# Performance work log

Hardware: AMD Instinct MI355X
Metric: run time of the kernel (lower is better)

Reference implementation:

```python
import jax, jax.numpy as jnp
import numpy as np

B, C_IN, C_OUT, N, K = 8, 64, 128, 2048, 16
EPS = 1e-5  # torch BatchNorm2d default


def setup_inputs() -> dict:
    key = jax.random.key(0)
    ks = jax.random.split(key, 2)
    x = jax.random.normal(ks[0], (B, C_IN, N, 1), dtype=jnp.float32)
    # Conv2d(2*C_IN, C_OUT, 1) kaiming_normal weight, zero bias; 1x1 kernel -> [C_OUT, 2*C_IN]
    W = jax.random.normal(ks[1], (C_OUT, 2 * C_IN), dtype=jnp.float32) * np.float32(np.sqrt(2.0 / (2 * C_IN)))
    b = jnp.zeros((C_OUT,), jnp.float32)
    gamma = jnp.ones((C_OUT,), jnp.float32)   # BN weight filled with 1
    beta = jnp.zeros((C_OUT,), jnp.float32)   # BN bias zeroed
    return {"x": x, "W": W, "b": b, "gamma": gamma, "beta": beta, "k": K}


def reference(x, W, b, gamma, beta, k):
    # x: [B, C, N, 1]
    xs = x[..., 0]                              # [B, C, N]
    feats = jnp.transpose(xs, (0, 2, 1))        # [B, N, C]
    # knn: pairwise_distance = -||xi||^2 + 2 xi.xj - ||xj||^2 (negative sq dist)
    sq = jnp.sum(xs * xs, axis=1)               # [B, N]
    gram = jnp.einsum('bcn,bcm->bnm', xs, xs)   # [B, N, N]
    pd = 2.0 * gram - sq[:, :, None] - sq[:, None, :]
    idx = jax.lax.top_k(pd, k)[1]               # [B, N, k] neighbor indices
    # gather: x_j = neighbor features, x_i = center features broadcast over k
    x_j = jnp.take_along_axis(feats[:, None, :, :], idx[:, :, :, None], axis=2)  # [B, N, k, C]
    x_i = feats[:, :, None, :]                  # [B, N, 1, C]
    e = jnp.concatenate([jnp.broadcast_to(x_i, x_j.shape), x_j - x_i], axis=-1)  # [B, N, k, 2C]
    # 1x1 conv (matmul over channels) + ReLU
    h = jax.nn.relu(jnp.einsum('bnkc,oc->bnko', e, W) + b)  # [B, N, k, O]
    # BatchNorm2d in training mode: batch stats over (B, N, k), biased variance
    mean = jnp.mean(h, axis=(0, 1, 2))
    var = jnp.mean(jnp.square(h - mean), axis=(0, 1, 2))
    h = (h - mean) * jax.lax.rsqrt(var + EPS) * gamma + beta
    # max over neighbors, back to [B, O, N, 1]
    out = jnp.max(h, axis=2)                    # [B, N, O]
    return jnp.transpose(out, (0, 2, 1))[..., None]
```

## Files before the change

### kernel.cpp

```cpp
#include <hip/hip_runtime.h>
#include <math.h>

#define BB 8
#define CIN 64
#define CO 128
#define NPT 2048
#define KK 16
#define EPSV 1e-5f
#define LOSCALE 2048.0f

typedef unsigned int u32;
typedef unsigned long long u64;
typedef _Float16 f16x8 __attribute__((ext_vector_type(8)));
typedef float f32x4 __attribute__((ext_vector_type(4)));

__global__ __launch_bounds__(256) void k_prep_pv(
    const float* __restrict__ x, const float* __restrict__ W,
    const float* __restrict__ bias, float* __restrict__ sq,
    _Float16* __restrict__ xh, _Float16* __restrict__ xl,
    float* __restrict__ p, float* __restrict__ v) {
  __shared__ float tile[64][65];
  __shared__ float tileT[64][68];
  __shared__ float psum[4][64];
  int bid = blockIdx.x;
  int b = bid >> 5;
  int n0 = (bid & 31) << 6;
  int tid = threadIdx.x;
  int q = tid >> 6, lo = tid & 63;
#pragma unroll
  for (int i = 0; i < 16; ++i) {
    int c = i * 4 + q;
    tile[c][lo] = x[((size_t)(b * CIN + c)) * NPT + n0 + lo];
  }
  __syncthreads();
  float ps = 0.f;
#pragma unroll
  for (int i = 0; i < 16; ++i) {
    float t = tile[q * 16 + i][lo];
    ps += t * t;
  }
  psum[q][lo] = ps;
#pragma unroll
  for (int i = 0; i < 16; ++i) {
    int ni = i * 4 + q;
    float val = tile[lo][ni];
    tileT[ni][lo] = val;
    size_t o = ((size_t)(b * NPT + n0 + ni)) * CIN + lo;
    _Float16 h = (_Float16)val;
    xh[o] = h;
    xl[o] = (_Float16)((val - (float)h) * LOSCALE);
  }
  __syncthreads();
  if (q == 0) {
    sq[(size_t)b * NPT + n0 + lo] = psum[0][lo] + psum[1][lo] + psum[2][lo] + psum[3][lo];
  }
  int o = tid & 127, hh = tid >> 7;
  const float4* W1 = (const float4*)&W[o * 2 * CIN];
  const float4* W2 = (const float4*)&W[o * 2 * CIN + CIN];
  float bo = bias[o];
#pragma unroll 2
  for (int t = 0; t < 32; ++t) {
    int node = t * 2 + hh;
    float a1 = 0.f, a2 = 0.f;
#pragma unroll
    for (int c4 = 0; c4 < 16; ++c4) {
      float4 xv = *(const float4*)&tileT[node][c4 * 4];
      float4 w1 = W1[c4];
      float4 w2 = W2[c4];
      a1 += xv.x * w1.x + xv.y * w1.y + xv.z * w1.z + xv.w * w1.w;
      a2 += xv.x * w2.x + xv.y * w2.y + xv.z * w2.z + xv.w * w2.w;
    }
    size_t gn = ((size_t)(b * NPT + n0 + node)) * CO + o;
    p[gn] = a1 - a2 + bo;
    v[gn] = a2;
  }
}

__global__ __launch_bounds__(1024) void k_dist_topk(
    const _Float16* __restrict__ xh, const _Float16* __restrict__ xl,
    const float* __restrict__ sq, int* __restrict__ idxout) {
  __shared__ uint4 tiles[16][2][256];
  __shared__ float submax[16][64];
  __shared__ float2 cand[16][96];
  __shared__ int cnt[16];
  __shared__ float tauf[16];

  int bid = (blockIdx.x & 7) * 128 + (blockIdx.x >> 3);
  int b = bid >> 7;
  int rt = (bid & 127) << 4;
  int tid = threadIdx.x;
  int w = tid >> 6, lane = tid & 63;
  int lr = lane & 15, lg = lane >> 4;
  const _Float16* xhb = xh + (size_t)b * NPT * CIN;
  const _Float16* xlb = xl + (size_t)b * NPT * CIN;
  const float* sqb = sq + (size_t)b * NPT;

  if (tid < 16) cnt[tid] = 0;

  const size_t arow = (size_t)(rt + lr) * CIN + lg * 8;
  f16x8 ah0 = *(const f16x8*)(xhb + arow);
  f16x8 ah1 = *(const f16x8*)(xhb + arow + 32);
  f16x8 al0 = *(const f16x8*)(xlb + arow);
  f16x8 al1 = *(const f16x8*)(xlb + arow + 32);
  float4 sqr = *(const float4*)(sqb + rt + lg * 4);
  float sqrv[4] = {sqr.x, sqr.y, sqr.z, sqr.w};
  float csqs[8];
#pragma unroll
  for (int t = 0; t < 8; ++t) csqs[t] = sqb[(w * 8 + t) * 16 + lr];

  const char* xhB = (const char*)xhb;
  const char* xlB = (const char*)xlb;
  const int su = (lane ^ ((lane >> 3) & 7)) * 16;

#define ISSUE_TILE(T)                                                          \
  {                                                                            \
    const int tb_ = (w * 8 + (T)) * 2048;                                      \
    uint4* buf_ = &tiles[w][(T) & 1][0];                                       \
    __builtin_amdgcn_global_load_lds((const uint4*)(xhB + tb_ + su),           \
                                     buf_, 16, 0, 0);                          \
    __builtin_amdgcn_global_load_lds((const uint4*)(xhB + tb_ + 1024 + su),    \
                                     buf_ + 64, 16, 0, 0);                     \
    __builtin_amdgcn_global_load_lds((const uint4*)(xlB + tb_ + su),           \
                                     buf_ + 128, 16, 0, 0);                    \
    __builtin_amdgcn_global_load_lds((const uint4*)(xlB + tb_ + 1024 + su),    \
                                     buf_ + 192, 16, 0, 0);                    \
  }

  ISSUE_TILE(0)
  ISSUE_TILE(1)

  const int uh0 = lr * 8 + (lg ^ (lr & 7));
  const int uh1 = lr * 8 + ((lg + 4) ^ (lr & 7));
  float vals[32];

#pragma unroll
  for (int t = 0; t < 8; ++t) {
    if (t < 7) { asm volatile("s_waitcnt vmcnt(4)" ::: "memory"); }
    else       { asm volatile("s_waitcnt vmcnt(0)" ::: "memory"); }
    __builtin_amdgcn_sched_barrier(0);
    const uint4* bufr = &tiles[w][t & 1][0];
    f16x8 bh0 = *(const f16x8*)(bufr + uh0);
    f16x8 bh1 = *(const f16x8*)(bufr + uh1);
    f16x8 bl0 = *(const f16x8*)(bufr + 128 + uh0);
    f16x8 bl1 = *(const f16x8*)(bufr + 128 + uh1);
    asm volatile("s_waitcnt lgkmcnt(0)" ::: "memory");
    __builtin_amdgcn_sched_barrier(0);
    if (t == 0) ISSUE_TILE(2)
    if (t == 1) ISSUE_TILE(3)
    if (t == 2) ISSUE_TILE(4)
    if (t == 3) ISSUE_TILE(5)
    if (t == 4) ISSUE_TILE(6)
    if (t == 5) ISSUE_TILE(7)
    f32x4 acc0 = {0.f, 0.f, 0.f, 0.f};
    f32x4 acc1 = {0.f, 0.f, 0.f, 0.f};
    acc1 = __builtin_amdgcn_mfma_f32_16x16x32_f16(ah0, bl0, acc1, 0, 0, 0);
    acc1 = __builtin_amdgcn_mfma_f32_16x16x32_f16(al0, bh0, acc1, 0, 0, 0);
    acc1 = __builtin_amdgcn_mfma_f32_16x16x32_f16(ah1, bl1, acc1, 0, 0, 0);
    acc1 = __builtin_amdgcn_mfma_f32_16x16x32_f16(al1, bh1, acc1, 0, 0, 0);
    acc0 = __builtin_amdgcn_mfma_f32_16x16x32_f16(ah0, bh0, acc0, 0, 0, 0);
    acc0 = __builtin_amdgcn_mfma_f32_16x16x32_f16(ah1, bh1, acc0, 0, 0, 0);
    const float k2 = 2.0f / LOSCALE;
#pragma unroll
    for (int q = 0; q < 4; ++q) {
      vals[t * 4 + q] = fmaf(acc1[q], k2, 2.f * acc0[q]) - (sqrv[q] + csqs[t]);
    }
  }
#undef ISSUE_TILE

  float rmax[4];
#pragma unroll
  for (int q = 0; q < 4; ++q) {
    float m = vals[q];
#pragma unroll
    for (int t = 1; t < 8; ++t) m = fmaxf(m, vals[t * 4 + q]);
    m = fmaxf(m, __shfl_xor(m, 1, 64));
    m = fmaxf(m, __shfl_xor(m, 2, 64));
    rmax[q] = m;
  }
  if ((lr & 3) == 0) {
    int pool = w * 4 + (lr >> 2);
#pragma unroll
    for (int q = 0; q < 4; ++q) submax[lg * 4 + q][pool] = rmax[q];
  }
  __syncthreads();

  {
    u32 ou = __float_as_uint(submax[w][lane]);
    ou = (ou & 0x80000000u) ? ~ou : (ou | 0x80000000u);
    u32 lo = 0u;
#pragma unroll
    for (int s2 = 31; s2 >= 16; --s2) {
      u32 cd = lo | (1u << s2);
      u64 bal = __ballot(ou >= cd);
      if (__popcll(bal) >= KK) lo = cd;
    }
    u32 tb = (lo & 0x80000000u) ? (lo ^ 0x80000000u) : ~lo;
    if (lane == 0) tauf[w] = __uint_as_float(tb);
  }
  __syncthreads();

  {
    float tq[4];
#pragma unroll
    for (int q = 0; q < 4; ++q) tq[q] = tauf[lg * 4 + q];
#pragma unroll
    for (int t = 0; t < 8; ++t) {
#pragma unroll
      for (int q = 0; q < 4; ++q) {
        float vv = vals[t * 4 + q];
        if (vv >= tq[q]) {
          int r = lg * 4 + q;
          int pos = atomicAdd(&cnt[r], 1);
          if (pos < 96) cand[r][pos] = make_float2(vv, __int_as_float((w * 8 + t) * 16 + lr));
        }
      }
    }
  }
  __syncthreads();

  int total = cnt[w];
  if (total > 96) total = 96;
  const float NINF = -__builtin_inff();
  float cv = NINF;
  int ci = 0x7FFFFFFF;
  int n1 = total < 64 ? total : 64;
  if (lane < n1) {
    float2 pr = cand[w][lane];
    cv = pr.x; ci = __float_as_int(pr.y);
  }

#define PSORT(KMAX)                                                        \
  _Pragma("unroll") for (int k = 2; k <= (KMAX); k <<= 1) {                \
    _Pragma("unroll") for (int j = k >> 1; j > 0; j >>= 1) {               \
      float pv = __shfl_xor(cv, j, 64);                                    \
      int pi = __shfl_xor(ci, j, 64);                                      \
      bool up = (lane & k) != 0;                                           \
      bool lw = (lane & j) == 0;                                           \
      bool gt = (cv > pv) || (cv == pv && ci < pi);                        \
      bool keep = (lw != up) ? gt : !gt;                                   \
      cv = keep ? cv : pv;                                                 \
      ci = keep ? ci : pi;                                                 \
    }                                                                      \
  }

  if (total > 32) {
    PSORT(64)
    if (total > 64) {
      if (lane >= 16) {
        int src2 = 48 + lane;
        if (src2 < total) {
          float2 pr = cand[w][src2];
          cv = pr.x; ci = __float_as_int(pr.y);
        } else { cv = NINF; ci = 0x7FFFFFFF; }
      }
      PSORT(64)
    }
  } else {
    PSORT(32)
  }
#undef PSORT

  if (lane < KK) idxout[((size_t)(b * NPT + rt + w)) * KK + lane] = ci;
}

__global__ __launch_bounds__(256) void k_stats(
    const float* __restrict__ p, const float* __restrict__ v,
    const int* __restrict__ idx, float* __restrict__ psums,
    float* __restrict__ psqs, float* __restrict__ mxb) {
  __shared__ float rs[8][CO];
  __shared__ float rq[8][CO];
  int bid = (blockIdx.x & 7) * 128 + (blockIdx.x >> 3);
  int b = bid >> 7;
  int n0 = (bid & 127) << 4;
  int tid = threadIdx.x;
  int o4 = tid & 31, ns = tid >> 5;
  const float* vb = v + (size_t)b * NPT * CO;
  float4 s = {0.f, 0.f, 0.f, 0.f};
  float4 qq = {0.f, 0.f, 0.f, 0.f};
#pragma unroll 1
  for (int g = 0; g < 2; ++g) {
    int gn = b * NPT + n0 + g * 8 + ns;
    size_t po = (size_t)gn * CO + o4 * 4;
    float4 p4 = *(const float4*)(p + po);
    const int* id = idx + (size_t)gn * KK;
    int4 j0 = *(const int4*)(id);
    int4 j1 = *(const int4*)(id + 4);
    int4 j2 = *(const int4*)(id + 8);
    int4 j3 = *(const int4*)(id + 12);
    int jj[16] = {j0.x, j0.y, j0.z, j0.w, j1.x, j1.y, j1.z, j1.w,
                  j2.x, j2.y, j2.z, j2.w, j3.x, j3.y, j3.z, j3.w};
    float4 mx4 = {-1e30f, -1e30f, -1e30f, -1e30f};
#pragma unroll
    for (int k = 0; k < KK; ++k) {
      float4 v4 = *(const float4*)(vb + (size_t)jj[k] * CO + o4 * 4);
      float h0 = fmaxf(p4.x + v4.x, 0.f);
      float h1 = fmaxf(p4.y + v4.y, 0.f);
      float h2 = fmaxf(p4.z + v4.z, 0.f);
      float h3 = fmaxf(p4.w + v4.w, 0.f);
      s.x += h0; s.y += h1; s.z += h2; s.w += h3;
      qq.x += h0 * h0; qq.y += h1 * h1; qq.z += h2 * h2; qq.w += h3 * h3;
      mx4.x = fmaxf(mx4.x, h0); mx4.y = fmaxf(mx4.y, h1);
      mx4.z = fmaxf(mx4.z, h2); mx4.w = fmaxf(mx4.w, h3);
    }
    *(float4*)(mxb + po) = mx4;
  }
  rs[ns][o4 * 4 + 0] = s.x;  rs[ns][o4 * 4 + 1] = s.y;
  rs[ns][o4 * 4 + 2] = s.z;  rs[ns][o4 * 4 + 3] = s.w;
  rq[ns][o4 * 4 + 0] = qq.x; rq[ns][o4 * 4 + 1] = qq.y;
  rq[ns][o4 * 4 + 2] = qq.z; rq[ns][o4 * 4 + 3] = qq.w;
  __syncthreads();
  if (tid < CO) {
    float ts = 0.f, tq = 0.f;
#pragma unroll
    for (int i = 0; i < 8; ++i) { ts += rs[i][tid]; tq += rq[i][tid]; }
    psums[(size_t)bid * CO + tid] = ts;
    psqs[(size_t)bid * CO + tid] = tq;
  }
}

__global__ __launch_bounds__(64) void k_final(
    const float* __restrict__ psums, const float* __restrict__ psqs,
    const float* __restrict__ gamma, const float* __restrict__ beta,
    float* __restrict__ scale, float* __restrict__ shift) {
  int o = blockIdx.x;
  int t = threadIdx.x;
  float s = 0.f, q = 0.f;
  for (int i = t; i < BB * (NPT / 16); i += 64) {
    s += psums[(size_t)i * CO + o];
    q += psqs[(size_t)i * CO + o];
  }
#pragma unroll
  for (int d = 32; d >= 1; d >>= 1) {
    s += __shfl_down(s, d, 64);
    q += __shfl_down(q, d, 64);
  }
  if (t == 0) {
    const float M = (float)(BB * NPT * KK);
    float mean = s / M;
    float var = q / M - mean * mean;
    float sc = gamma[o] * rsqrtf(var + EPSV);
    scale[o] = sc;
    shift[o] = beta[o] - mean * sc;
  }
}

__global__ __launch_bounds__(256) void k_out_fast(
    const float* __restrict__ mxb, const float* __restrict__ scale,
    const float* __restrict__ shift, float* __restrict__ out) {
  __shared__ float ob[32][132];
  int bid = blockIdx.x;
  int b = bid >> 6;
  int n0 = (bid & 63) << 5;
  int tid = threadIdx.x;
  int o4 = tid & 31, ns = tid >> 5;
  float4 sc = *(const float4*)(scale + o4 * 4);
  float4 sh = *(const float4*)(shift + o4 * 4);
#pragma unroll
  for (int g = 0; g < 4; ++g) {
    int node = g * 8 + ns;
    size_t po = (size_t)(b * NPT + n0 + node) * CO + o4 * 4;
    float4 mx = *(const float4*)(mxb + po);
    float4 r;
    r.x = mx.x * sc.x + sh.x;
    r.y = mx.y * sc.y + sh.y;
    r.z = mx.z * sc.z + sh.z;
    r.w = mx.w * sc.w + sh.w;
    *(float4*)&ob[node][o4 * 4] = r;
  }
  __syncthreads();
  int ni = tid & 31, oh = tid >> 5;
#pragma unroll
  for (int pass = 0; pass < 16; ++pass) {
    int o = pass * 8 + oh;
    out[((size_t)(b * CO + o)) * NPT + n0 + ni] = ob[ni][o];
  }
}

extern "C" void kernel_launch(void* const* d_in, const int* in_sizes, int n_in,
                              void* d_out, int out_size, void* d_ws, size_t ws_size,
                              hipStream_t stream) {
  const float* x = (const float*)d_in[0];
  const float* W = (const float*)d_in[1];
  const float* bias = (const float*)d_in[2];
  const float* gamma = (const float*)d_in[3];
  const float* beta = (const float*)d_in[4];
  float* out = (float*)d_out;

  char* ws = (char*)d_ws;
  size_t off = 0;
  auto alloc = [&](size_t bytes) {
    void* ptr = ws + off;
    off += (bytes + 255) & ~(size_t)255;
    return ptr;
  };
  float* ft = (float*)alloc(sizeof(float) * BB * NPT * CIN);
  _Float16* xh = (_Float16*)alloc(sizeof(_Float16) * BB * NPT * CIN);
  _Float16* xl = (_Float16*)alloc(sizeof(_Float16) * BB * NPT * CIN);
  float* mx = ft;
  float* sq = (float*)alloc(sizeof(float) * BB * NPT);
  float* p = (float*)alloc(sizeof(float) * BB * NPT * CO);
  float* v = (float*)alloc(sizeof(float) * BB * NPT * CO);
  int* idx = (int*)alloc(sizeof(int) * BB * NPT * KK);
  float* psums = (float*)alloc(sizeof(float) * BB * (NPT / 16) * CO);
  float* psqs = (float*)alloc(sizeof(float) * BB * (NPT / 16) * CO);
  float* scale = (float*)alloc(sizeof(float) * CO);
  float* shift = (float*)alloc(sizeof(float) * CO);
  (void)ws_size; (void)in_sizes; (void)n_in; (void)out_size;

  hipLaunchKernelGGL(k_prep_pv, dim3(BB * (NPT / 64)), dim3(256), 0, stream,
                     x, W, bias, sq, xh, xl, p, v);
  hipLaunchKernelGGL(k_dist_topk, dim3(BB * (NPT / 16)), dim3(1024), 0, stream, xh, xl, sq, idx);
  hipLaunchKernelGGL(k_stats, dim3(BB * (NPT / 16)), dim3(256), 0, stream, p, v, idx, psums, psqs, mx);
  hipLaunchKernelGGL(k_final, dim3(CO), dim3(64), 0, stream, psums, psqs, gamma, beta, scale, shift);
  hipLaunchKernelGGL(k_out_fast, dim3(BB * (NPT / 32)), dim3(256), 0, stream, mx, scale, shift, out);
}
```

Measured before the change: 108.8 us.

## Fuse neighbor gather, ReLU and BN statistics into the top-k kernel

Removes the separate stats kernel. Each wave in the distance/top-k kernel shuffles its own top-k indices across lanes, gathers the neighbor v rows and computes ReLU sums, squared sums and the max in place. The max result overwrites p in place, and the per-block partial sums are reduced through the reused shared tile buffer. This drops the idx round trip through global memory and one kernel launch. In exchange, the gather work now runs inside a 1024-thread kernel with heavy shared-memory use.

```diff
diff --git a/kernel.cpp b/kernel.cpp
--- a/kernel.cpp
+++ b/kernel.cpp
@@ -78,7 +78,9 @@
 
 __global__ __launch_bounds__(1024) void k_dist_topk(
     const _Float16* __restrict__ xh, const _Float16* __restrict__ xl,
-    const float* __restrict__ sq, int* __restrict__ idxout) {
+    const float* __restrict__ sq, float* p_mx,
+    const float* __restrict__ v, float* __restrict__ psums,
+    float* __restrict__ psqs) {
   __shared__ uint4 tiles[16][2][256];
   __shared__ float submax[16][64];
   __shared__ float2 cand[16][96];
@@ -260,61 +262,37 @@
   }
 #undef PSORT
 
-  if (lane < KK) idxout[((size_t)(b * NPT + rt + w)) * KK + lane] = ci;
-}
-
-__global__ __launch_bounds__(256) void k_stats(
-    const float* __restrict__ p, const float* __restrict__ v,
-    const int* __restrict__ idx, float* __restrict__ psums,
-    float* __restrict__ psqs, float* __restrict__ mxb) {
-  __shared__ float rs[8][CO];
-  __shared__ float rq[8][CO];
-  int bid = (blockIdx.x & 7) * 128 + (blockIdx.x >> 3);
-  int b = bid >> 7;
-  int n0 = (bid & 127) << 4;
-  int tid = threadIdx.x;
-  int o4 = tid & 31, ns = tid >> 5;
-  const float* vb = v + (size_t)b * NPT * CO;
-  float4 s = {0.f, 0.f, 0.f, 0.f};
-  float4 qq = {0.f, 0.f, 0.f, 0.f};
-#pragma unroll 1
-  for (int g = 0; g < 2; ++g) {
-    int gn = b * NPT + n0 + g * 8 + ns;
-    size_t po = (size_t)gn * CO + o4 * 4;
-    float4 p4 = *(const float4*)(p + po);
-    const int* id = idx + (size_t)gn * KK;
-    int4 j0 = *(const int4*)(id);
-    int4 j1 = *(const int4*)(id + 4);
-    int4 j2 = *(const int4*)(id + 8);
-    int4 j3 = *(const int4*)(id + 12);
-    int jj[16] = {j0.x, j0.y, j0.z, j0.w, j1.x, j1.y, j1.z, j1.w,
-                  j2.x, j2.y, j2.z, j2.w, j3.x, j3.y, j3.z, j3.w};
-    float4 mx4 = {-1e30f, -1e30f, -1e30f, -1e30f};
+  {
+    int jj[16];
+#pragma unroll
+    for (int k = 0; k < KK; ++k) jj[k] = __shfl(ci, k, 64) & (NPT - 1);
+    size_t gn = (size_t)(b * NPT + rt + w);
+    const float* vb = v + (size_t)b * NPT * CO;
+    float2 p2 = *(const float2*)(p_mx + gn * CO + lane * 2);
+    float2 s2 = {0.f, 0.f}, q2 = {0.f, 0.f}, m2 = {-1e30f, -1e30f};
 #pragma unroll
     for (int k = 0; k < KK; ++k) {
-      float4 v4 = *(const float4*)(vb + (size_t)jj[k] * CO + o4 * 4);
-      float h0 = fmaxf(p4.x + v4.x, 0.f);
-      float h1 = fmaxf(p4.y + v4.y, 0.f);
-      float h2 = fmaxf(p4.z + v4.z, 0.f);
-      float h3 = fmaxf(p4.w + v4.w, 0.f);
-      s.x += h0; s.y += h1; s.z += h2; s.w += h3;
-      qq.x += h0 * h0; qq.y += h1 * h1; qq.z += h2 * h2; qq.w += h3 * h3;
-      mx4.x = fmaxf(mx4.x, h0); mx4.y = fmaxf(mx4.y, h1);
-      mx4.z = fmaxf(mx4.z, h2); mx4.w = fmaxf(mx4.w, h3);
-    }
-    *(float4*)(mxb + po) = mx4;
-  }
-  rs[ns][o4 * 4 + 0] = s.x;  rs[ns][o4 * 4 + 1] = s.y;
-  rs[ns][o4 * 4 + 2] = s.z;  rs[ns][o4 * 4 + 3] = s.w;
-  rq[ns][o4 * 4 + 0] = qq.x; rq[ns][o4 * 4 + 1] = qq.y;
-  rq[ns][o4 * 4 + 2] = qq.z; rq[ns][o4 * 4 + 3] = qq.w;
+      float2 v2 = *(const float2*)(vb + (size_t)jj[k] * CO + lane * 2);
+      float h0 = fmaxf(p2.x + v2.x, 0.f);
+      float h1 = fmaxf(p2.y + v2.y, 0.f);
+      s2.x += h0; s2.y += h1;
+      q2.x += h0 * h0; q2.y += h1 * h1;
+      m2.x = fmaxf(m2.x, h0); m2.y = fmaxf(m2.y, h1);
+    }
+    *(float2*)(p_mx + gn * CO + lane * 2) = m2;
+    float* sp = (float*)tiles;
+    *(float2*)(sp + w * 128 + lane * 2) = s2;
+    *(float2*)(sp + 2048 + w * 128 + lane * 2) = q2;
+  }
   __syncthreads();
   if (tid < CO) {
+    float* sp = (float*)tiles;
     float ts = 0.f, tq = 0.f;
 #pragma unroll
-    for (int i = 0; i < 8; ++i) { ts += rs[i][tid]; tq += rq[i][tid]; }
-    psums[(size_t)bid * CO + tid] = ts;
-    psqs[(size_t)bid * CO + tid] = tq;
+    for (int i = 0; i < 16; ++i) { ts += sp[i * 128 + tid]; tq += sp[2048 + i * 128 + tid]; }
+    int obid = b * 128 + (rt >> 4);
+    psums[(size_t)obid * CO + tid] = ts;
+    psqs[(size_t)obid * CO + tid] = tq;
   }
 }
 
@@ -393,14 +371,11 @@
     off += (bytes + 255) & ~(size_t)255;
     return ptr;
   };
-  float* ft = (float*)alloc(sizeof(float) * BB * NPT * CIN);
   _Float16* xh = (_Float16*)alloc(sizeof(_Float16) * BB * NPT * CIN);
   _Float16* xl = (_Float16*)alloc(sizeof(_Float16) * BB * NPT * CIN);
-  float* mx = ft;
   float* sq = (float*)alloc(sizeof(float) * BB * NPT);
   float* p = (float*)alloc(sizeof(float) * BB * NPT * CO);
   float* v = (float*)alloc(sizeof(float) * BB * NPT * CO);
-  int* idx = (int*)alloc(sizeof(int) * BB * NPT * KK);
   float* psums = (float*)alloc(sizeof(float) * BB * (NPT / 16) * CO);
   float* psqs = (float*)alloc(sizeof(float) * BB * (NPT / 16) * CO);
   float* scale = (float*)alloc(sizeof(float) * CO);
@@ -409,8 +384,8 @@
 
   hipLaunchKernelGGL(k_prep_pv, dim3(BB * (NPT / 64)), dim3(256), 0, stream,
                      x, W, bias, sq, xh, xl, p, v);
-  hipLaunchKernelGGL(k_dist_topk, dim3(BB * (NPT / 16)), dim3(1024), 0, stream, xh, xl, sq, idx);
-  hipLaunchKernelGGL(k_stats, dim3(BB * (NPT / 16)), dim3(256), 0, stream, p, v, idx, psums, psqs, mx);
+  hipLaunchKernelGGL(k_dist_topk, dim3(BB * (NPT / 16)), dim3(1024), 0, stream,
+                     xh, xl, sq, p, v, psums, psqs);
   hipLaunchKernelGGL(k_final, dim3(CO), dim3(64), 0, stream, psums, psqs, gamma, beta, scale, shift);
-  hipLaunchKernelGGL(k_out_fast, dim3(BB * (NPT / 32)), dim3(256), 0, stream, mx, scale, shift, out);
-}
+  hipLaunchKernelGGL(k_out_fast, dim3(BB * (NPT / 32)), dim3(256), 0, stream, p, scale, shift, out);
+}
```

After: 107.4 us. Within noise of the previous version (-1.3%).
